# Optimization experiments

Hardware: AMD Instinct MI355X
Metric: run time of the kernel (lower is better)

The kernel has to match this reference:

```python
import jax, jax.numpy as jnp
import numpy as np

N, E, D, H = 50000, 500000, 160, 5
C = D // H          # per-head channels = 32
MLP_H = 50          # hidden_dim of output MLP
NEG_SLOPE = 0.2
EPS = 1e-5


def layer_norm(x, g, b):
    mu = jnp.mean(x, axis=-1, keepdims=True)
    var = jnp.mean((x - mu) ** 2, axis=-1, keepdims=True)
    return (x - mu) / jnp.sqrt(var + EPS) * g + b


def setup_inputs() -> dict:
    key = jax.random.key(0)
    ks = jax.random.split(key, 24)
    s_d = 1.0 / np.sqrt(D)
    s_h = 1.0 / np.sqrt(MLP_H)
    inp = {
        "x": jax.random.normal(ks[0], (N, D), jnp.float32),
        "edge_index": jax.random.randint(ks[1], (2, E), 0, N, jnp.int32),
        "edge_attr": jax.random.normal(ks[2], (E, D), jnp.float32),
        "u": jax.random.normal(ks[3], (1, 16), jnp.float32),
        "batch": jnp.zeros((N,), jnp.int32),
        # GATv2Conv params (lin_l, lin_r, lin_edge, att, out bias)
        "Wl": jax.random.normal(ks[4], (D, H * C), jnp.float32) * s_d,
        "bl": jnp.zeros((H * C,), jnp.float32),
        "Wr": jax.random.normal(ks[5], (D, H * C), jnp.float32) * s_d,
        "br": jnp.zeros((H * C,), jnp.float32),
        "We": jax.random.normal(ks[6], (D, H * C), jnp.float32) * s_d,
        "att": jax.random.normal(ks[7], (H, C), jnp.float32) * (1.0 / np.sqrt(C)),
        "bias": jnp.zeros((H * C,), jnp.float32),
        # norm1
        "g1": jnp.ones((D,), jnp.float32),
        "beta1": jnp.zeros((D,), jnp.float32),
        # output MLP: Linear(D,50) -> SELU -> LN(50) -> Linear(50,D)
        "W1": jax.random.normal(ks[8], (D, MLP_H), jnp.float32) * s_d,
        "b1": jnp.zeros((MLP_H,), jnp.float32),
        "gm": jnp.ones((MLP_H,), jnp.float32),
        "bm": jnp.zeros((MLP_H,), jnp.float32),
        "W2": jax.random.normal(ks[9], (MLP_H, D), jnp.float32) * s_h,
        "b2": jnp.zeros((D,), jnp.float32),
        # norm2
        "g2": jnp.ones((D,), jnp.float32),
        "beta2": jnp.zeros((D,), jnp.float32),
    }
    return inp


def gatv2(x, edge_index, edge_attr, Wl, bl, Wr, br, We, att, bias):
    src, dst = edge_index[0], edge_index[1]
    xl = (x @ Wl + bl).reshape(N, H, C)   # source transform (x_j)
    xr = (x @ Wr + br).reshape(N, H, C)   # target transform (x_i)
    ea = (edge_attr @ We).reshape(E, H, C)
    m = xl[src] + xr[dst] + ea            # [E,H,C]
    score = jnp.einsum('ehc,hc->eh', jax.nn.leaky_relu(m, NEG_SLOPE), att)  # [E,H]
    # softmax over incoming edges of each destination node
    smax = jax.ops.segment_max(score, dst, num_segments=N)  # [N,H]
    sexp = jnp.exp(score - smax[dst])
    ssum = jax.ops.segment_sum(sexp, dst, num_segments=N)   # [N,H]
    alpha = sexp / jnp.where(ssum == 0.0, 1.0, ssum)[dst]   # [E,H]
    out = jax.ops.segment_sum(xl[src] * alpha[:, :, None], dst, num_segments=N)
    return out.reshape(N, H * C) + bias


def reference(x, edge_index, edge_attr, u, batch,
              Wl, bl, Wr, br, We, att, bias,
              g1, beta1, W1, b1, gm, bm, W2, b2, g2, beta2):
    attn = gatv2(x, edge_index, edge_attr, Wl, bl, Wr, br, We, att, bias)
    h = layer_norm(x + attn, g1, beta1)
    mlp = layer_norm(jax.nn.selu(h @ W1 + b1), gm, bm) @ W2 + b2
    return layer_norm(h + mlp, g2, beta2)
```

## Files before the change

### kernel.cpp

```cpp
#include <hip/hip_runtime.h>

#define NNODES 50000
#define NEDGES 500000
#define DIM    160
#define NHEAD  5
#define MLPH   50

typedef __bf16 bf16x8 __attribute__((ext_vector_type(8)));
typedef float  f32x4  __attribute__((ext_vector_type(4)));

#define PB_WLT   0
#define PB_WRT   25600
#define PB_WET   51200
#define PB_W1    76800
#define PB_W2    84800
#define PB_VEC   92800
#define PB_SMALL 94240
#define PB_TOTAL 94400

struct Ptrs {
    const void *Wl, *Wr, *We;
    const void *bl, *br, *att, *bias, *g1, *beta1;
    const void *W1, *b1, *gm, *bm, *W2, *b2, *g2, *beta2;
};

__device__ __forceinline__ float ldany(const void* p, long i, bool f32) {
    return f32 ? ((const float*)p)[i] : (float)(((const __bf16*)p)[i]);
}

__global__ void detect_kernel(const unsigned short* __restrict__ xs, int* __restrict__ flag) {
    __shared__ int red[4];
    int cnt = 0;
    for (int i = threadIdx.x; i < 65536; i += 256) {
        unsigned e = (xs[i] >> 7) & 0xFFu;
        if (e >= 137u) cnt++;
    }
    for (int off = 1; off < 64; off <<= 1) cnt += __shfl_xor(cnt, off, 64);
    if ((threadIdx.x & 63) == 0) red[threadIdx.x >> 6] = cnt;
    __syncthreads();
    if (threadIdx.x == 0) flag[0] = (red[0] + red[1] + red[2] + red[3] > 1000) ? 1 : 0;
}

__global__ void prep_kernel(Ptrs p, __bf16* __restrict__ pb, const int* __restrict__ flag) {
    const bool f32 = flag[0] != 0;
    int i = blockIdx.x * 256 + threadIdx.x;
    if (i < 76800) {
        int which = i / 25600, r = i - which * 25600;
        int n = r / DIM, k = r - n * DIM;
        const void* w = which == 0 ? p.Wl : which == 1 ? p.Wr : p.We;
        pb[i] = (__bf16)ldany(w, (long)k * DIM + n, f32);
    } else if (i < 84800) {
        pb[i] = (__bf16)ldany(p.W1, i - PB_W1, f32);
    } else if (i < 92800) {
        pb[i] = (__bf16)ldany(p.W2, i - PB_W2, f32);
    } else if (i < 94240) {
        int t = i - PB_VEC, which = t / DIM, off = t - which * DIM;
        const void* v = which == 0 ? p.bl : which == 1 ? p.br : which == 2 ? p.att :
                        which == 3 ? p.bias : which == 4 ? p.g1 : which == 5 ? p.beta1 :
                        which == 6 ? p.b2 : which == 7 ? p.g2 : p.beta2;
        pb[i] = (__bf16)ldany(v, off, f32);
    } else if (i < 94390) {
        int t = i - PB_SMALL;
        const void* v = t < 50 ? p.b1 : t < 100 ? p.gm : p.bm;
        pb[i] = (__bf16)ldany(v, t % 50, f32);
    }
}

template <bool DO_SCORE>
__global__ __launch_bounds__(256, 3) void gemm160(
    const void* __restrict__ A, long M,
    const __bf16* __restrict__ Bt,
    const __bf16* __restrict__ bias,
    __bf16* __restrict__ Cout,
    const __bf16* __restrict__ xl, const __bf16* __restrict__ xr,
    const int* __restrict__ src, const int* __restrict__ dst,
    const __bf16* __restrict__ att, float* __restrict__ score,
    int* __restrict__ cursor, int* __restrict__ psrc,
    const int* __restrict__ flag)
{
    constexpr int BROW = 168;
    __shared__ __bf16 Bts[DIM * BROW];
    const bool aF32 = flag[0] != 0;
    const int tid  = threadIdx.x;
    const int wave = tid >> 6, lane = tid & 63;
    const int quad = lane >> 4, l16 = lane & 15;
    const long blockRow = (long)blockIdx.x * 128;

    long row0 = blockRow + wave * 32 + l16;
    long row1 = row0 + 16;
    const long cr0 = row0 < M ? row0 : M - 1;
    const long cr1 = row1 < M ? row1 : M - 1;

    const f32x4 zero4 = {0.f, 0.f, 0.f, 0.f};
    f32x4 acc[2][10];
#pragma unroll
    for (int r = 0; r < 2; r++)
#pragma unroll
        for (int n = 0; n < 10; n++) acc[r][n] = zero4;

    if (aF32) {
        const float* A0 = (const float*)A + cr0 * DIM + quad * 8;
        const float* A1 = (const float*)A + cr1 * DIM + quad * 8;
        float4 buf[2][2][2];
        buf[0][0][0] = *(const float4*)(A0);
        buf[0][0][1] = *(const float4*)(A0 + 4);
        buf[0][1][0] = *(const float4*)(A1);
        buf[0][1][1] = *(const float4*)(A1 + 4);
        for (int i = tid; i < DIM * DIM / 8; i += 256) {
            int row = i / 20, c = i - row * 20;
            *(uint4*)(Bts + row * BROW + c * 8) = ((const uint4*)Bt)[i];
        }
        __syncthreads();
#pragma unroll
        for (int kk = 0; kk < 5; kk++) {
            const int k0 = kk * 32;
            if (kk < 4) {
                buf[(kk + 1) & 1][0][0] = *(const float4*)(A0 + k0 + 32);
                buf[(kk + 1) & 1][0][1] = *(const float4*)(A0 + k0 + 36);
                buf[(kk + 1) & 1][1][0] = *(const float4*)(A1 + k0 + 32);
                buf[(kk + 1) & 1][1][1] = *(const float4*)(A1 + k0 + 36);
            }
            bf16x8 a0, a1;
            {
                float4 f0 = buf[kk & 1][0][0], f1 = buf[kk & 1][0][1];
                a0[0] = (__bf16)f0.x; a0[1] = (__bf16)f0.y;
                a0[2] = (__bf16)f0.z; a0[3] = (__bf16)f0.w;
                a0[4] = (__bf16)f1.x; a0[5] = (__bf16)f1.y;
                a0[6] = (__bf16)f1.z; a0[7] = (__bf16)f1.w;
                f0 = buf[kk & 1][1][0]; f1 = buf[kk & 1][1][1];
                a1[0] = (__bf16)f0.x; a1[1] = (__bf16)f0.y;
                a1[2] = (__bf16)f0.z; a1[3] = (__bf16)f0.w;
                a1[4] = (__bf16)f1.x; a1[5] = (__bf16)f1.y;
                a1[6] = (__bf16)f1.z; a1[7] = (__bf16)f1.w;
            }
#pragma unroll
            for (int n = 0; n < 10; n++) {
                bf16x8 b = *(const bf16x8*)(Bts + (n * 16 + l16) * BROW + k0 + quad * 8);
                acc[0][n] = __builtin_amdgcn_mfma_f32_16x16x32_bf16(a0, b, acc[0][n], 0, 0, 0);
                acc[1][n] = __builtin_amdgcn_mfma_f32_16x16x32_bf16(a1, b, acc[1][n], 0, 0, 0);
            }
        }
    } else {
        const __bf16* A0 = (const __bf16*)A + cr0 * DIM + quad * 8;
        const __bf16* A1 = (const __bf16*)A + cr1 * DIM + quad * 8;
        bf16x8 af[5][2];
#pragma unroll
        for (int kk = 0; kk < 5; kk++) {
            af[kk][0] = *(const bf16x8*)(A0 + kk * 32);
            af[kk][1] = *(const bf16x8*)(A1 + kk * 32);
        }
        for (int i = tid; i < DIM * DIM / 8; i += 256) {
            int row = i / 20, c = i - row * 20;
            *(uint4*)(Bts + row * BROW + c * 8) = ((const uint4*)Bt)[i];
        }
        __syncthreads();
#pragma unroll
        for (int kk = 0; kk < 5; kk++) {
            const int k0 = kk * 32;
#pragma unroll
            for (int n = 0; n < 10; n++) {
                bf16x8 b = *(const bf16x8*)(Bts + (n * 16 + l16) * BROW + k0 + quad * 8);
                acc[0][n] = __builtin_amdgcn_mfma_f32_16x16x32_bf16(af[kk][0], b, acc[0][n], 0, 0, 0);
                acc[1][n] = __builtin_amdgcn_mfma_f32_16x16x32_bf16(af[kk][1], b, acc[1][n], 0, 0, 0);
            }
        }
    }

    if (!DO_SCORE) {
#pragma unroll
        for (int r = 0; r < 2; r++)
#pragma unroll
            for (int n = 0; n < 10; n++) {
                int col = n * 16 + l16;
                float bv = (float)bias[col];
#pragma unroll
                for (int reg = 0; reg < 4; reg++) {
                    long row = blockRow + wave * 32 + r * 16 + quad * 4 + reg;
                    if (row < M) Cout[row * DIM + col] = (__bf16)(acc[r][n][reg] + bv);
                }
            }
    } else {
#pragma unroll
        for (int r = 0; r < 2; r++) {
            long erow[4]; int sv[4], dv[4]; int slot[4] = {0, 0, 0, 0};
#pragma unroll
            for (int reg = 0; reg < 4; reg++) {
                erow[reg] = blockRow + wave * 32 + r * 16 + quad * 4 + reg;
                long e = erow[reg] < M ? erow[reg] : M - 1;
                sv[reg] = src[e]; dv[reg] = dst[e];
            }
            if (l16 == 0) {
#pragma unroll
                for (int reg = 0; reg < 4; reg++)
                    if (erow[reg] < M) slot[reg] = atomicAdd(&cursor[dv[reg]], 1);
            }
#pragma unroll
            for (int hh = 0; hh < NHEAD; hh++) {
                float sacc[4] = {0.f, 0.f, 0.f, 0.f};
#pragma unroll
                for (int sub = 0; sub < 2; sub++) {
                    int n = hh * 2 + sub;
                    int col = n * 16 + l16;
                    float av = (float)att[col];
#pragma unroll
                    for (int reg = 0; reg < 4; reg++) {
                        float m = acc[r][n][reg]
                                + (float)xl[(long)sv[reg] * DIM + col]
                                + (float)xr[(long)dv[reg] * DIM + col];
                        m = m > 0.f ? m : 0.2f * m;
                        sacc[reg] += m * av;
                    }
                }
#pragma unroll
                for (int off = 1; off < 16; off <<= 1)
#pragma unroll
                    for (int reg = 0; reg < 4; reg++)
                        sacc[reg] += __shfl_xor(sacc[reg], off, 64);
                if (l16 == 0) {
#pragma unroll
                    for (int reg = 0; reg < 4; reg++)
                        if (erow[reg] < M) score[(long)slot[reg] * NHEAD + hh] = sacc[reg];
                }
            }
            if (l16 == 0) {
#pragma unroll
                for (int reg = 0; reg < 4; reg++)
                    if (erow[reg] < M) psrc[slot[reg]] = sv[reg];
            }
        }
    }
}

__global__ void hist_kernel(const int* __restrict__ dst, int* __restrict__ deg) {
    int e = blockIdx.x * 256 + threadIdx.x;
    if (e < NEDGES) atomicAdd(&deg[dst[e]], 1);
}

__global__ __launch_bounds__(1024) void scan_kernel(const int* __restrict__ deg,
                                                    int* __restrict__ offs,
                                                    int* __restrict__ cursor) {
    __shared__ int part[1024];
    const int t = threadIdx.x;
    const int chunk = (NNODES + 1023) / 1024;
    int beg = t * chunk;
    int end = beg + chunk;
    if (beg > NNODES) beg = NNODES;
    if (end > NNODES) end = NNODES;
    int s = 0;
    for (int i = beg; i < end; i++) s += deg[i];
    part[t] = s;
    __syncthreads();
    for (int off = 1; off < 1024; off <<= 1) {
        int v = 0;
        if (t >= off) v = part[t - off];
        __syncthreads();
        part[t] += v;
        __syncthreads();
    }
    int run = (t == 0) ? 0 : part[t - 1];
    for (int i = beg; i < end; i++) {
        offs[i] = run; cursor[i] = run;
        run += deg[i];
    }
    if (t == 1023) offs[NNODES] = run;
}

__global__ __launch_bounds__(256) void node_kernel(
    const int* __restrict__ offs, const int* __restrict__ psrc,
    const float* __restrict__ score,
    const __bf16* __restrict__ xl, const void* __restrict__ x,
    const __bf16* __restrict__ pb, const int* __restrict__ flag,
    __bf16* __restrict__ hout)
{
    const bool f32 = flag[0] != 0;
    const __bf16* bias  = pb + PB_VEC + 3 * DIM;
    const __bf16* g1    = pb + PB_VEC + 4 * DIM;
    const __bf16* beta1 = pb + PB_VEC + 5 * DIM;
    const int lane = threadIdx.x & 63;
    const long n = (long)blockIdx.x * 4 + (threadIdx.x >> 6);
    const int beg = offs[n], end = offs[n + 1];
    const int deg = end - beg;

    float mx[NHEAD];
#pragma unroll
    for (int h = 0; h < NHEAD; h++) mx[h] = -1e30f;
    for (int j = lane; j < deg; j += 64) {
        const float* sp = score + (long)(beg + j) * NHEAD;
#pragma unroll
        for (int h = 0; h < NHEAD; h++) mx[h] = fmaxf(mx[h], sp[h]);
    }
#pragma unroll
    for (int h = 0; h < NHEAD; h++)
#pragma unroll
        for (int off = 1; off < 64; off <<= 1)
            mx[h] = fmaxf(mx[h], __shfl_xor(mx[h], off, 64));

    float sm[NHEAD] = {0.f, 0.f, 0.f, 0.f, 0.f};
    float accv[3] = {0.f, 0.f, 0.f};
    for (int j0 = 0; j0 < deg; j0 += 64) {
        const int cn = min(deg - j0, 64);
        float w[NHEAD]; int si = 0;
        if (lane < cn) {
            const float* sp = score + (long)(beg + j0 + lane) * NHEAD;
#pragma unroll
            for (int h = 0; h < NHEAD; h++) {
                w[h] = expf(sp[h] - mx[h]);
                sm[h] += w[h];
            }
            si = psrc[beg + j0 + lane];
        } else {
#pragma unroll
            for (int h = 0; h < NHEAD; h++) w[h] = 0.f;
        }
        for (int j = 0; j < cn; j++) {
            const int sj = __shfl(si, j, 64);
            const float w0 = __shfl(w[0], j, 64);
            const float w1 = __shfl(w[1], j, 64);
            const float w2 = __shfl(w[2], j, 64);
            const float w3 = __shfl(w[3], j, 64);
            const float w4 = __shfl(w[4], j, 64);
            const __bf16* xrow = xl + (long)sj * DIM;
            accv[0] += (lane < 32 ? w0 : w1) * (float)xrow[lane];
            accv[1] += (lane < 32 ? w2 : w3) * (float)xrow[lane + 64];
            if (lane < 32) accv[2] += w4 * (float)xrow[lane + 128];
        }
    }
#pragma unroll
    for (int h = 0; h < NHEAD; h++)
#pragma unroll
        for (int off = 1; off < 64; off <<= 1)
            sm[h] += __shfl_xor(sm[h], off, 64);
    float ism[NHEAD];
#pragma unroll
    for (int h = 0; h < NHEAD; h++) ism[h] = sm[h] > 0.f ? 1.f / sm[h] : 0.f;
    accv[0] *= lane < 32 ? ism[0] : ism[1];
    accv[1] *= lane < 32 ? ism[2] : ism[3];
    accv[2] *= ism[4];

    const int nch = (lane < 32) ? 3 : 2;
    float v[3]; float s1 = 0.f, s2 = 0.f;
    for (int c = 0; c < nch; c++) {
        int ch = lane + c * 64;
        float xv = f32 ? ((const float*)x)[n * DIM + ch]
                       : (float)(((const __bf16*)x)[n * DIM + ch]);
        float t = accv[c] + (float)bias[ch] + xv;
        v[c] = t; s1 += t; s2 += t * t;
    }
    for (int off = 1; off < 64; off <<= 1) {
        s1 += __shfl_xor(s1, off, 64);
        s2 += __shfl_xor(s2, off, 64);
    }
    float mu = s1 * (1.f / DIM);
    float var = fmaxf(s2 * (1.f / DIM) - mu * mu, 0.f);
    float rs = rsqrtf(var + 1e-5f);
    for (int c = 0; c < nch; c++) {
        int ch = lane + c * 64;
        hout[n * DIM + ch] = (__bf16)((v[c] - mu) * rs * (float)g1[ch] + (float)beta1[ch]);
    }
}

__global__ __launch_bounds__(256, 2) void mlp_kernel(
    const __bf16* __restrict__ hmat, const __bf16* __restrict__ pb,
    float* __restrict__ out)
{
    __shared__ __bf16 W1s[DIM * MLPH];
    __shared__ __bf16 W2s[MLPH * DIM];
    __shared__ float hrow[4][DIM];
    __shared__ float zrow[4][MLPH];
    const __bf16* W1 = pb + PB_W1;
    const __bf16* W2 = pb + PB_W2;
    const __bf16* b2 = pb + PB_VEC + 6 * DIM;
    const __bf16* g2 = pb + PB_VEC + 7 * DIM;
    const __bf16* beta2 = pb + PB_VEC + 8 * DIM;
    const __bf16* b1 = pb + PB_SMALL;
    const __bf16* gm = pb + PB_SMALL + 50;
    const __bf16* bm = pb + PB_SMALL + 100;
    const int tid = threadIdx.x, wave = tid >> 6, lane = tid & 63;
    for (int i = tid; i < DIM * MLPH / 8; i += 256) {
        ((uint4*)W1s)[i] = ((const uint4*)W1)[i];
        ((uint4*)W2s)[i] = ((const uint4*)W2)[i];
    }
    __syncthreads();
    const int nch = (lane < 32) ? 3 : 2;
    for (int it = 0; it < 4; it++) {
        long n = (long)blockIdx.x * 16 + it * 4 + wave;
        float hv[3];
        for (int c = 0; c < nch; c++) {
            int ch = lane + c * 64;
            float t = (float)hmat[n * DIM + ch];
            hv[c] = t; hrow[wave][ch] = t;
        }
        __syncthreads();
        float z = 0.f;
        if (lane < MLPH) {
            z = (float)b1[lane];
            for (int k = 0; k < DIM; k++) z += hrow[wave][k] * (float)W1s[k * MLPH + lane];
            const float SC = 1.0507009873554805f, AL = 1.6732632423543772f;
            z = (z > 0.f) ? SC * z : SC * AL * (expf(z) - 1.f);
        }
        float s1 = (lane < MLPH) ? z : 0.f, s2 = (lane < MLPH) ? z * z : 0.f;
        for (int off = 1; off < 64; off <<= 1) {
            s1 += __shfl_xor(s1, off, 64);
            s2 += __shfl_xor(s2, off, 64);
        }
        float mu = s1 * (1.f / MLPH);
        float var = fmaxf(s2 * (1.f / MLPH) - mu * mu, 0.f);
        float rs = rsqrtf(var + 1e-5f);
        if (lane < MLPH) zrow[wave][lane] = (z - mu) * rs * (float)gm[lane] + (float)bm[lane];
        __syncthreads();
        float y[3], t1 = 0.f, t2 = 0.f;
        for (int c = 0; c < nch; c++) {
            int ch = lane + c * 64;
            float o = (float)b2[ch];
            for (int j = 0; j < MLPH; j++) o += zrow[wave][j] * (float)W2s[j * DIM + ch];
            float yy = hv[c] + o;
            y[c] = yy; t1 += yy; t2 += yy * yy;
        }
        for (int off = 1; off < 64; off <<= 1) {
            t1 += __shfl_xor(t1, off, 64);
            t2 += __shfl_xor(t2, off, 64);
        }
        float mu2 = t1 * (1.f / DIM);
        float var2 = fmaxf(t2 * (1.f / DIM) - mu2 * mu2, 0.f);
        float rs2 = rsqrtf(var2 + 1e-5f);
        for (int c = 0; c < nch; c++) {
            int ch = lane + c * 64;
            out[n * DIM + ch] = (y[c] - mu2) * rs2 * (float)g2[ch] + (float)beta2[ch];
        }
        __syncthreads();
    }
}

extern "C" void kernel_launch(void* const* d_in, const int* in_sizes, int n_in,
                              void* d_out, int out_size, void* d_ws, size_t ws_size,
                              hipStream_t stream)
{
    const void* x   = d_in[0];
    const int*  ei  = (const int*)d_in[1];
    const void* ea  = d_in[2];
    Ptrs p;
    p.Wl = d_in[5];  p.bl = d_in[6];  p.Wr = d_in[7];  p.br = d_in[8];
    p.We = d_in[9];  p.att = d_in[10]; p.bias = d_in[11];
    p.g1 = d_in[12]; p.beta1 = d_in[13];
    p.W1 = d_in[14]; p.b1 = d_in[15]; p.gm = d_in[16]; p.bm = d_in[17];
    p.W2 = d_in[18]; p.b2 = d_in[19]; p.g2 = d_in[20]; p.beta2 = d_in[21];
    const int* srcp = ei;
    const int* dstp = ei + NEDGES;

    char* ws = (char*)d_ws;
    int*    flag   = (int*)ws;    ws += 16;
    __bf16* pb     = (__bf16*)ws; ws += (size_t)PB_TOTAL * 2;
    int*    deg    = (int*)ws;    ws += (size_t)NNODES * 4;
    int*    offs   = (int*)ws;    ws += (size_t)(NNODES + 1) * 4 + 12;
    int*    cursor = (int*)ws;    ws += (size_t)NNODES * 4;
    int*    psrc   = (int*)ws;    ws += (size_t)NEDGES * 4;
    float*  score  = (float*)ws;  ws += (size_t)NEDGES * NHEAD * 4;
    __bf16* xl     = (__bf16*)ws; ws += (size_t)NNODES * DIM * 2;
    __bf16* xr     = (__bf16*)ws; ws += (size_t)NNODES * DIM * 2;
    __bf16* hbuf   = xr;
    const size_t NEEDED = (size_t)(ws - (char*)d_ws);

    if (ws_size < NEEDED) {
        return;
    }

    (void)hipMemsetAsync(deg, 0, (size_t)NNODES * 4, stream);

    detect_kernel<<<1, 256, 0, stream>>>((const unsigned short*)x, flag);
    prep_kernel<<<369, 256, 0, stream>>>(p, pb, flag);

    const int gemmN = (NNODES + 127) / 128;
    const int gemmE = (NEDGES + 127) / 128;
    gemm160<false><<<gemmN, 256, 0, stream>>>(x, NNODES, pb + PB_WLT, pb + PB_VEC + 0 * DIM, xl,
                                              nullptr, nullptr, nullptr, nullptr, nullptr, nullptr,
                                              nullptr, nullptr, flag);
    gemm160<false><<<gemmN, 256, 0, stream>>>(x, NNODES, pb + PB_WRT, pb + PB_VEC + 1 * DIM, xr,
                                              nullptr, nullptr, nullptr, nullptr, nullptr, nullptr,
                                              nullptr, nullptr, flag);

    hist_kernel<<<(NEDGES + 255) / 256, 256, 0, stream>>>(dstp, deg);
    scan_kernel<<<1, 1024, 0, stream>>>(deg, offs, cursor);

    gemm160<true><<<gemmE, 256, 0, stream>>>(ea, NEDGES, pb + PB_WET, nullptr, nullptr,
                                             xl, xr, srcp, dstp, pb + PB_VEC + 2 * DIM, score,
                                             cursor, psrc, flag);

    node_kernel<<<NNODES / 4, 256, 0, stream>>>(offs, psrc, score, xl, x, pb, flag, hbuf);

    mlp_kernel<<<NNODES / 16, 256, 0, stream>>>(hbuf, pb, (float*)d_out);
}
```

Before: 1.056 ms.

## Sort edges by destination before edge GEMM and gather edge_attr via permutation

```diff
diff --git a/kernel.cpp b/kernel.cpp
--- a/kernel.cpp
+++ b/kernel.cpp
@@ -73,9 +73,9 @@
     const __bf16* __restrict__ bias,
     __bf16* __restrict__ Cout,
     const __bf16* __restrict__ xl, const __bf16* __restrict__ xr,
-    const int* __restrict__ src, const int* __restrict__ dst,
+    const int* __restrict__ perm, const int* __restrict__ psrc,
+    const int* __restrict__ dst,
     const __bf16* __restrict__ att, float* __restrict__ score,
-    int* __restrict__ cursor, int* __restrict__ psrc,
     const int* __restrict__ flag)
 {
     constexpr int BROW = 168;
@@ -90,6 +90,13 @@
     long row1 = row0 + 16;
     const long cr0 = row0 < M ? row0 : M - 1;
     const long cr1 = row1 < M ? row1 : M - 1;
+    long ar0 = cr0, ar1 = cr1;
+    if (DO_SCORE) { ar0 = perm[cr0]; ar1 = perm[cr1]; }
+
+    for (int i = tid; i < DIM * DIM / 8; i += 256) {
+        int row = i / 20, c = i - row * 20;
+        *(uint4*)(Bts + row * BROW + c * 8) = ((const uint4*)Bt)[i];
+    }
 
     const f32x4 zero4 = {0.f, 0.f, 0.f, 0.f};
     f32x4 acc[2][10];
@@ -99,17 +106,13 @@
         for (int n = 0; n < 10; n++) acc[r][n] = zero4;
 
     if (aF32) {
-        const float* A0 = (const float*)A + cr0 * DIM + quad * 8;
-        const float* A1 = (const float*)A + cr1 * DIM + quad * 8;
+        const float* A0 = (const float*)A + ar0 * DIM + quad * 8;
+        const float* A1 = (const float*)A + ar1 * DIM + quad * 8;
         float4 buf[2][2][2];
         buf[0][0][0] = *(const float4*)(A0);
         buf[0][0][1] = *(const float4*)(A0 + 4);
         buf[0][1][0] = *(const float4*)(A1);
         buf[0][1][1] = *(const float4*)(A1 + 4);
-        for (int i = tid; i < DIM * DIM / 8; i += 256) {
-            int row = i / 20, c = i - row * 20;
-            *(uint4*)(Bts + row * BROW + c * 8) = ((const uint4*)Bt)[i];
-        }
         __syncthreads();
 #pragma unroll
         for (int kk = 0; kk < 5; kk++) {
@@ -141,17 +144,13 @@
             }
         }
     } else {
-        const __bf16* A0 = (const __bf16*)A + cr0 * DIM + quad * 8;
-        const __bf16* A1 = (const __bf16*)A + cr1 * DIM + quad * 8;
+        const __bf16* A0 = (const __bf16*)A + ar0 * DIM + quad * 8;
+        const __bf16* A1 = (const __bf16*)A + ar1 * DIM + quad * 8;
         bf16x8 af[5][2];
 #pragma unroll
         for (int kk = 0; kk < 5; kk++) {
             af[kk][0] = *(const bf16x8*)(A0 + kk * 32);
             af[kk][1] = *(const bf16x8*)(A1 + kk * 32);
-        }
-        for (int i = tid; i < DIM * DIM / 8; i += 256) {
-            int row = i / 20, c = i - row * 20;
-            *(uint4*)(Bts + row * BROW + c * 8) = ((const uint4*)Bt)[i];
         }
         __syncthreads();
 #pragma unroll
@@ -182,17 +181,13 @@
     } else {
 #pragma unroll
         for (int r = 0; r < 2; r++) {
-            long erow[4]; int sv[4], dv[4]; int slot[4] = {0, 0, 0, 0};
+            long erow[4]; int sv[4], dv[4];
 #pragma unroll
             for (int reg = 0; reg < 4; reg++) {
                 erow[reg] = blockRow + wave * 32 + r * 16 + quad * 4 + reg;
                 long e = erow[reg] < M ? erow[reg] : M - 1;
-                sv[reg] = src[e]; dv[reg] = dst[e];
-            }
-            if (l16 == 0) {
-#pragma unroll
-                for (int reg = 0; reg < 4; reg++)
-                    if (erow[reg] < M) slot[reg] = atomicAdd(&cursor[dv[reg]], 1);
+                sv[reg] = psrc[e];
+                dv[reg] = dst[perm[e]];
             }
 #pragma unroll
             for (int hh = 0; hh < NHEAD; hh++) {
@@ -219,13 +214,8 @@
                 if (l16 == 0) {
 #pragma unroll
                     for (int reg = 0; reg < 4; reg++)
-                        if (erow[reg] < M) score[(long)slot[reg] * NHEAD + hh] = sacc[reg];
+                        if (erow[reg] < M) score[erow[reg] * NHEAD + hh] = sacc[reg];
                 }
-            }
-            if (l16 == 0) {
-#pragma unroll
-                for (int reg = 0; reg < 4; reg++)
-                    if (erow[reg] < M) psrc[slot[reg]] = sv[reg];
             }
         }
     }
@@ -263,6 +253,17 @@
         run += deg[i];
     }
     if (t == 1023) offs[NNODES] = run;
+}
+
+__global__ void fill_kernel(const int* __restrict__ src, const int* __restrict__ dst,
+                            int* __restrict__ cursor, int* __restrict__ perm,
+                            int* __restrict__ psrc) {
+    int e = blockIdx.x * 256 + threadIdx.x;
+    if (e < NEDGES) {
+        int p = atomicAdd(&cursor[dst[e]], 1);
+        perm[p] = e;
+        psrc[p] = src[e];
+    }
 }
 
 __global__ __launch_bounds__(256) void node_kernel(
@@ -453,6 +454,7 @@
     int*    deg    = (int*)ws;    ws += (size_t)NNODES * 4;
     int*    offs   = (int*)ws;    ws += (size_t)(NNODES + 1) * 4 + 12;
     int*    cursor = (int*)ws;    ws += (size_t)NNODES * 4;
+    int*    perm   = (int*)ws;    ws += (size_t)NEDGES * 4;
     int*    psrc   = (int*)ws;    ws += (size_t)NEDGES * 4;
     float*  score  = (float*)ws;  ws += (size_t)NEDGES * NHEAD * 4;
     __bf16* xl     = (__bf16*)ws; ws += (size_t)NNODES * DIM * 2;
@@ -472,18 +474,19 @@
     const int gemmN = (NNODES + 127) / 128;
     const int gemmE = (NEDGES + 127) / 128;
     gemm160<false><<<gemmN, 256, 0, stream>>>(x, NNODES, pb + PB_WLT, pb + PB_VEC + 0 * DIM, xl,
-                                              nullptr, nullptr, nullptr, nullptr, nullptr, nullptr,
+                                              nullptr, nullptr, nullptr, nullptr, nullptr,
                                               nullptr, nullptr, flag);
     gemm160<false><<<gemmN, 256, 0, stream>>>(x, NNODES, pb + PB_WRT, pb + PB_VEC + 1 * DIM, xr,
-                                              nullptr, nullptr, nullptr, nullptr, nullptr, nullptr,
+                                              nullptr, nullptr, nullptr, nullptr, nullptr,
                                               nullptr, nullptr, flag);
 
     hist_kernel<<<(NEDGES + 255) / 256, 256, 0, stream>>>(dstp, deg);
     scan_kernel<<<1, 1024, 0, stream>>>(deg, offs, cursor);
+    fill_kernel<<<(NEDGES + 255) / 256, 256, 0, stream>>>(srcp, dstp, cursor, perm, psrc);
 
     gemm160<true><<<gemmE, 256, 0, stream>>>(ea, NEDGES, pb + PB_WET, nullptr, nullptr,
-                                             xl, xr, srcp, dstp, pb + PB_VEC + 2 * DIM, score,
-                                             cursor, psrc, flag);
+                                             xl, xr, perm, psrc, dstp,
+                                             pb + PB_VEC + 2 * DIM, score, flag);
 
     node_kernel<<<NNODES / 4, 256, 0, stream>>>(offs, psrc, score, xl, x, pb, flag, hbuf);
 
```

Result: no change. 1.051 ms (-0.4%).
